# Kernel tuning notes

Measured on AMD Instinct MI355X. Metric: run time of the kernel, lower is better.

## Reference

```python
import jax, jax.numpy as jnp
import numpy as np

D_MODEL = 1024
N_HEADS = 16
HEAD_DIM = 64
SEQ = 2048
BATCH = 2
NEG = -1e9


def rotate_half(t):
    t1, t2 = jnp.split(t, 2, axis=-1)
    return jnp.concatenate([-t2, t1], axis=-1)


def setup_inputs() -> dict:
    key = jax.random.key(0)
    ks = jax.random.split(key, 7)
    std = 0.02
    x = jax.random.normal(ks[0], (BATCH, SEQ, D_MODEL), dtype=jnp.float32)
    # RoPE tables [seq_len, head_dim]
    inv_freq = 1.0 / (10000.0 ** (jnp.arange(0, HEAD_DIM, 2, dtype=jnp.float32) / HEAD_DIM))
    t = jnp.arange(SEQ, dtype=jnp.float32)
    freqs = jnp.outer(t, inv_freq)
    emb = jnp.concatenate([freqs, freqs], axis=-1)
    cos = jnp.cos(emb)
    sin = jnp.sin(emb)
    Wq = std * jax.random.normal(ks[1], (D_MODEL, D_MODEL), dtype=jnp.float32)
    Wk = std * jax.random.normal(ks[2], (D_MODEL, D_MODEL), dtype=jnp.float32)
    Wv = std * jax.random.normal(ks[3], (D_MODEL, D_MODEL), dtype=jnp.float32)
    Wo = std * jax.random.normal(ks[4], (D_MODEL, D_MODEL), dtype=jnp.float32)
    return {"x": x, "cos": cos, "sin": sin, "Wq": Wq, "Wk": Wk, "Wv": Wv, "Wo": Wo}


def reference(x, cos, sin, Wq, Wk, Wv, Wo):
    B, S, _ = x.shape
    scale = 1.0 / np.sqrt(HEAD_DIM)
    # projections (nn.Linear: y = x @ W.T)
    q = (x @ Wq.T).reshape(B, S, N_HEADS, HEAD_DIM).transpose(0, 2, 1, 3)  # [B,H,S,D]
    k = (x @ Wk.T).reshape(B, S, N_HEADS, HEAD_DIM).transpose(0, 2, 1, 3)
    v = (x @ Wv.T).reshape(B, S, N_HEADS, HEAD_DIM).transpose(0, 2, 1, 3)
    # RoPE
    c = cos[None, None, :, :]
    s = sin[None, None, :, :]
    q = q * c + rotate_half(q) * s
    k = k * c + rotate_half(k) * s
    # attention with additive causal mask
    scores = jnp.einsum('bhqd,bhkd->bhqk', q, k) * scale
    causal = jnp.triu(jnp.ones((S, S), dtype=jnp.float32), k=1) * NEG
    scores = scores + causal[None, None]
    attn = jax.nn.softmax(scores, axis=-1)
    out = jnp.einsum('bhqk,bhkd->bhqd', attn, v)
    out = out.transpose(0, 2, 1, 3).reshape(B, S, D_MODEL)
    return out @ Wo.T
```

## Files before the change

### kernel.cpp

```cpp
#include <hip/hip_runtime.h>
#include <hip/hip_bf16.h>
#include <math.h>

#define DM    1024
#define SEQL  2048
#define NB    2
#define MTOT  4096

typedef __attribute__((ext_vector_type(8))) short short8;
typedef __attribute__((ext_vector_type(4))) short short4v;
typedef __attribute__((ext_vector_type(4))) float float4v;

#define GLDS16(g, l) __builtin_amdgcn_global_load_lds( \
    (const __attribute__((address_space(1))) void*)(g), \
    (__attribute__((address_space(3))) void*)(l), 16, 0, 0)

__device__ __forceinline__ short f2bf(float f) {
  union { float f; unsigned u; } c; c.f = f;
  unsigned r = c.u + 0x7FFFu + ((c.u >> 16) & 1u);
  return (short)(r >> 16);
}

__global__ __launch_bounds__(256) void cvt_all(
    const float* __restrict__ x, const float* __restrict__ wq, const float* __restrict__ wk,
    const float* __restrict__ wv, const float* __restrict__ wo,
    short* __restrict__ xb, short* __restrict__ wqb, short* __restrict__ wkb,
    short* __restrict__ wvb, short* __restrict__ wob) {
  const int n4x = MTOT * DM / 4;
  int i = blockIdx.x * 256 + threadIdx.x;
  const float* s; short* d; int off;
  if (i < n4x) { s = x; d = xb; off = i; }
  else {
    int j = i - n4x;
    int sel = j >> 18;
    off = j & 0x3FFFF;
    s = (sel == 0) ? wq : (sel == 1) ? wk : (sel == 2) ? wv : wo;
    d = (sel == 0) ? wqb : (sel == 1) ? wkb : (sel == 2) ? wvb : wob;
  }
  float4 v = ((const float4*)s)[off];
  short4v o;
  o.x = f2bf(v.x); o.y = f2bf(v.y); o.z = f2bf(v.z); o.w = f2bf(v.w);
  ((short4v*)d)[off] = o;
}

template<int MODE>
__global__ __launch_bounds__(256, 2) void gemm_kernel(
    const short* __restrict__ A,
    const short* __restrict__ B0, const short* __restrict__ B1, const short* __restrict__ B2,
    void* __restrict__ out0, void* __restrict__ out1, void* __restrict__ out2,
    const float* __restrict__ cosp, const float* __restrict__ sinp)
{
  __shared__ short As[128 * 32];
  __shared__ short Bs[128 * 32];
  const int t = threadIdx.x;
  const int w = t >> 6, lane = t & 63;
  const int quad = lane >> 4, l16 = lane & 15;
  const int wm = w >> 1, wn = w & 1;
  const int bm = blockIdx.y * 128, bn = blockIdx.x * 128;

  const short* Bw;
  if (MODE == 2) Bw = B0;
  else Bw = (blockIdx.z == 0) ? B0 : ((blockIdx.z == 1) ? B1 : B2);

  float4v acc[4][4];
#pragma unroll
  for (int i = 0; i < 4; ++i)
#pragma unroll
    for (int j = 0; j < 4; ++j) { float4v z = {0.f, 0.f, 0.f, 0.f}; acc[i][j] = z; }

  for (int k0 = 0; k0 < DM; k0 += 32) {
#pragma unroll
    for (int i = 0; i < 2; ++i) {
      const int c = i * 256 + t;
      const int row = c >> 2, kc = c & 3;
      GLDS16(A  + (size_t)(bm + row) * DM + k0 + kc * 8, As + (i * 256 + w * 64) * 8);
      GLDS16(Bw + (size_t)(bn + row) * DM + k0 + kc * 8, Bs + (i * 256 + w * 64) * 8);
    }
    __syncthreads();
    short8 af[4], bf[4];
#pragma unroll
    for (int mt = 0; mt < 4; ++mt) af[mt] = *(const short8*)&As[(wm * 64 + mt * 16 + l16) * 32 + quad * 8];
#pragma unroll
    for (int nt = 0; nt < 4; ++nt) bf[nt] = *(const short8*)&Bs[(wn * 64 + nt * 16 + l16) * 32 + quad * 8];
#pragma unroll
    for (int mt = 0; mt < 4; ++mt)
#pragma unroll
      for (int nt = 0; nt < 4; ++nt)
        acc[mt][nt] = __builtin_amdgcn_mfma_f32_16x16x32_bf16(af[mt], bf[nt], acc[mt][nt], 0, 0, 0);
    __syncthreads();
  }

  if (MODE == 2) {
    float* fo = (float*)out0;
#pragma unroll
    for (int mt = 0; mt < 4; ++mt)
#pragma unroll
      for (int nt = 0; nt < 4; ++nt)
#pragma unroll
        for (int r = 0; r < 4; ++r) {
          int grow = bm + wm * 64 + mt * 16 + quad * 4 + r;
          int gcol = bn + wn * 64 + nt * 16 + l16;
          fo[(size_t)grow * DM + gcol] = acc[mt][nt][r];
        }
  } else if (blockIdx.z < 2) {
    short* qo = (short*)((blockIdx.z == 0) ? out0 : out1);
    const float sc = (blockIdx.z == 0) ? 0.125f : 1.0f;
#pragma unroll
    for (int mt = 0; mt < 4; ++mt)
#pragma unroll
      for (int r = 0; r < 4; ++r) {
        int grow = bm + wm * 64 + mt * 16 + quad * 4 + r;
        int s = grow & (SEQL - 1);
        int base = grow * DM + bn + wn * 64;
#pragma unroll
        for (int nt = 0; nt < 2; ++nt) {
          int d1 = nt * 16 + l16;
          float q1 = acc[mt][nt][r], q2 = acc[mt][nt + 2][r];
          float c1 = cosp[s * 64 + d1] * sc,      s1 = sinp[s * 64 + d1] * sc;
          float c2 = cosp[s * 64 + 32 + d1] * sc, s2 = sinp[s * 64 + 32 + d1] * sc;
          qo[base + d1]      = f2bf(q1 * c1 - q2 * s1);
          qo[base + 32 + d1] = f2bf(q2 * c2 + q1 * s2);
        }
      }
  } else {
    short* vo = (short*)out2;
#pragma unroll
    for (int mt = 0; mt < 4; ++mt)
#pragma unroll
      for (int nt = 0; nt < 4; ++nt) {
        int gc = bn + wn * 64 + nt * 16 + l16;
        int g0 = bm + wm * 64 + mt * 16 + quad * 4;
        short4v pk;
#pragma unroll
        for (int r = 0; r < 4; ++r) pk[r] = f2bf(acc[mt][nt][r]);
        *(short4v*)&vo[(size_t)gc * MTOT + g0] = pk;
      }
  }
}

__device__ __forceinline__ void softmax_pv(
    float4v* __restrict__ sA, float* __restrict__ lrun, float4v* __restrict__ o,
    short* __restrict__ Pw, const short* __restrict__ Vs,
    int qt, int kt, bool maskit, int w, int quad, int l16)
{
#pragma unroll
  for (int r = 0; r < 4; ++r) {
    int qrow = qt * 64 + w * 16 + quad * 4 + r;
#pragma unroll
    for (int nt = 0; nt < 8; ++nt) {
      float p;
      if (maskit && (kt * 128 + nt * 16 + l16 > qrow)) p = 0.f;
      else p = __expf(sA[nt][r]);
      lrun[r] += p;
      Pw[(quad * 4 + r) * 136 + nt * 16 + l16] = f2bf(p);
    }
  }
#pragma unroll
  for (int kk = 0; kk < 4; ++kk) {
    short8 ap = *(const short8*)&Pw[l16 * 136 + kk * 32 + quad * 8];
#pragma unroll
    for (int nt = 0; nt < 4; ++nt) {
      int d = nt * 16 + l16;
      short8 bv = *(const short8*)&Vs[(d * 16 + ((kk * 4 + quad) ^ (d & 7))) * 8];
      o[nt] = __builtin_amdgcn_mfma_f32_16x16x32_bf16(ap, bv, o[nt], 0, 0, 0);
    }
  }
}

__global__ __launch_bounds__(256, 2) void attn_kernel(
    const short* __restrict__ Q, const short* __restrict__ K,
    const short* __restrict__ Vt, short* __restrict__ O)
{
  __shared__ short Ks[128 * 64];
  __shared__ short Vs[64 * 128];
  __shared__ short Pl[4 * 16 * 136];
  const int t = threadIdx.x;
  const int w = t >> 6, lane = t & 63;
  const int quad = lane >> 4, l16 = lane & 15;
  const int qtA = blockIdx.x;
  const int qtB = 31 - blockIdx.x;
  const int bh = blockIdx.y;
  const int b = bh >> 4, h = bh & 15;
  const int rowbase = b * SEQL;
  const int colbase = h * 64;
  const int nktA = (qtA >> 1) + 1;
  const int nktB = (qtB >> 1) + 1;
  short* Pw = &Pl[w * 16 * 136];

  short8 aqA[2], aqB[2];
#pragma unroll
  for (int kk = 0; kk < 2; ++kk) {
    int rA = rowbase + qtA * 64 + w * 16 + l16;
    int rB = rowbase + qtB * 64 + w * 16 + l16;
    aqA[kk] = *(const short8*)&Q[(size_t)rA * DM + colbase + kk * 32 + quad * 8];
    aqB[kk] = *(const short8*)&Q[(size_t)rB * DM + colbase + kk * 32 + quad * 8];
  }

  float4v oA[4], oB[4];
  float lA[4], lB[4];
#pragma unroll
  for (int j = 0; j < 4; ++j) {
    float4v z = {0.f, 0.f, 0.f, 0.f};
    oA[j] = z; oB[j] = z; lA[j] = 0.f; lB[j] = 0.f;
  }

  for (int kt = 0; kt < nktB; ++kt) {
    const bool actA = (kt < nktA);
    {
      const short* Kbase = K + (size_t)(rowbase + kt * 128) * DM + colbase;
      const short* Vbase = Vt + (size_t)colbase * MTOT + rowbase + kt * 128;
#pragma unroll
      for (int j = 0; j < 4; ++j) {
        int i = j * 256 + t;
        int n = i >> 3, c = (i & 7) ^ (n & 7);
        GLDS16(Kbase + (size_t)n * DM + c * 8, Ks + (j * 256 + w * 64) * 8);
      }
#pragma unroll
      for (int j = 0; j < 4; ++j) {
        int i = j * 256 + t;
        int d = i >> 4, c = (i & 15) ^ (d & 7);
        GLDS16(Vbase + (size_t)d * MTOT + c * 8, Vs + (j * 256 + w * 64) * 8);
      }
    }
    __syncthreads();

    float4v sAa[8], sAb[8];
#pragma unroll
    for (int j = 0; j < 8; ++j) { float4v z = {0.f, 0.f, 0.f, 0.f}; sAa[j] = z; sAb[j] = z; }
    if (actA) {
#pragma unroll
      for (int nt = 0; nt < 8; ++nt) {
        int n = nt * 16 + l16;
        short8 bk0 = *(const short8*)&Ks[(n * 8 + (quad ^ (n & 7))) * 8];
        short8 bk1 = *(const short8*)&Ks[(n * 8 + ((4 + quad) ^ (n & 7))) * 8];
        sAa[nt] = __builtin_amdgcn_mfma_f32_16x16x32_bf16(aqA[0], bk0, sAa[nt], 0, 0, 0);
        sAa[nt] = __builtin_amdgcn_mfma_f32_16x16x32_bf16(aqA[1], bk1, sAa[nt], 0, 0, 0);
        sAb[nt] = __builtin_amdgcn_mfma_f32_16x16x32_bf16(aqB[0], bk0, sAb[nt], 0, 0, 0);
        sAb[nt] = __builtin_amdgcn_mfma_f32_16x16x32_bf16(aqB[1], bk1, sAb[nt], 0, 0, 0);
      }
    } else {
#pragma unroll
      for (int nt = 0; nt < 8; ++nt) {
        int n = nt * 16 + l16;
        short8 bk0 = *(const short8*)&Ks[(n * 8 + (quad ^ (n & 7))) * 8];
        short8 bk1 = *(const short8*)&Ks[(n * 8 + ((4 + quad) ^ (n & 7))) * 8];
        sAb[nt] = __builtin_amdgcn_mfma_f32_16x16x32_bf16(aqB[0], bk0, sAb[nt], 0, 0, 0);
        sAb[nt] = __builtin_amdgcn_mfma_f32_16x16x32_bf16(aqB[1], bk1, sAb[nt], 0, 0, 0);
      }
    }

    if (actA) softmax_pv(sAa, lA, oA, Pw, Vs, qtA, kt, kt == nktA - 1, w, quad, l16);
    softmax_pv(sAb, lB, oB, Pw, Vs, qtB, kt, kt == nktB - 1, w, quad, l16);
    __syncthreads();
  }

#pragma unroll
  for (int r = 0; r < 4; ++r) {
#pragma unroll
    for (int off = 1; off < 16; off <<= 1) {
      lA[r] += __shfl_xor(lA[r], off);
      lB[r] += __shfl_xor(lB[r], off);
    }
  }
#pragma unroll
  for (int nt = 0; nt < 4; ++nt)
#pragma unroll
    for (int r = 0; r < 4; ++r) {
      int gcol = colbase + nt * 16 + l16;
      int growA = rowbase + qtA * 64 + w * 16 + quad * 4 + r;
      int growB = rowbase + qtB * 64 + w * 16 + quad * 4 + r;
      O[(size_t)growA * DM + gcol] = f2bf(oA[nt][r] / lA[r]);
      O[(size_t)growB * DM + gcol] = f2bf(oB[nt][r] / lB[r]);
    }
}

extern "C" void kernel_launch(void* const* d_in, const int* in_sizes, int n_in,
                              void* d_out, int out_size, void* d_ws, size_t ws_size,
                              hipStream_t stream) {
  const float* x    = (const float*)d_in[0];
  const float* cosp = (const float*)d_in[1];
  const float* sinp = (const float*)d_in[2];
  const float* Wq   = (const float*)d_in[3];
  const float* Wk   = (const float*)d_in[4];
  const float* Wv   = (const float*)d_in[5];
  const float* Wo   = (const float*)d_in[6];

  char* ws = (char*)d_ws;
  const size_t XB = (size_t)MTOT * DM * 2;
  const size_t WB = (size_t)DM * DM * 2;
  short* xb    = (short*)(ws);
  short* wqb   = (short*)(ws + XB);
  short* wkb   = (short*)(ws + XB + 1 * WB);
  short* wvb   = (short*)(ws + XB + 2 * WB);
  short* wob   = (short*)(ws + XB + 3 * WB);
  short* Qb    = (short*)(ws + XB + 4 * WB);
  short* Kb    = (short*)(ws + XB + 4 * WB + XB);
  short* Vtb   = (short*)(ws + XB + 4 * WB + 2 * XB);
  short* attnb = xb;

  const int n4tot = (MTOT * DM + 4 * DM * DM) / 4;
  hipLaunchKernelGGL(cvt_all, dim3(n4tot / 256), dim3(256), 0, stream,
                     x, Wq, Wk, Wv, Wo, xb, wqb, wkb, wvb, wob);

  hipLaunchKernelGGL((gemm_kernel<0>), dim3(DM / 128, MTOT / 128, 3), dim3(256), 0, stream,
                     xb, wqb, wkb, wvb, (void*)Qb, (void*)Kb, (void*)Vtb, cosp, sinp);

  hipLaunchKernelGGL(attn_kernel, dim3(16, NB * 16), dim3(256), 0, stream,
                     Qb, Kb, Vtb, attnb);

  hipLaunchKernelGGL((gemm_kernel<2>), dim3(DM / 128, MTOT / 128, 1), dim3(256), 0, stream,
                     attnb, wob, wob, wob, d_out, nullptr, nullptr, cosp, sinp);
}
```

Before: 190.4 us.

## Keep softmax probabilities in registers, use exp2 scaling, split output GEMM tiles

The attention kernel computes S transposed (K as the A operand) so that each lane holds probabilities for its own query column. It packs them to bf16 in registers and feeds them straight into a 16x16x16 MFMA against V, dropping the LDS round-trip for P and one sync per tile. The Q scale folds in log2(e) so exp2 replaces expf, and the row sum becomes a single scalar reduced with two shuffles. The output projection gets its own kernel with 128x64 tiles to double the block count, and the QKV GEMM raises its occupancy hint to 3. The packbf helper rounds half-up instead of round-to-nearest-even, a small numerical difference.

```diff
diff --git a/kernel.cpp b/kernel.cpp
--- a/kernel.cpp
+++ b/kernel.cpp
@@ -19,6 +19,11 @@
   union { float f; unsigned u; } c; c.f = f;
   unsigned r = c.u + 0x7FFFu + ((c.u >> 16) & 1u);
   return (short)(r >> 16);
+}
+
+__device__ __forceinline__ int packbf(float a, float b) {
+  union { float f; unsigned u; } ca, cb; ca.f = a; cb.f = b;
+  return (int)__builtin_amdgcn_perm(cb.u + 0x8000u, ca.u + 0x8000u, 0x07060302u);
 }
 
 __global__ __launch_bounds__(256) void cvt_all(
@@ -43,11 +48,10 @@
   ((short4v*)d)[off] = o;
 }
 
-template<int MODE>
-__global__ __launch_bounds__(256, 2) void gemm_kernel(
+__global__ __launch_bounds__(256, 3) void qkv_kernel(
     const short* __restrict__ A,
     const short* __restrict__ B0, const short* __restrict__ B1, const short* __restrict__ B2,
-    void* __restrict__ out0, void* __restrict__ out1, void* __restrict__ out2,
+    short* __restrict__ out0, short* __restrict__ out1, short* __restrict__ out2,
     const float* __restrict__ cosp, const float* __restrict__ sinp)
 {
   __shared__ short As[128 * 32];
@@ -58,9 +62,7 @@
   const int wm = w >> 1, wn = w & 1;
   const int bm = blockIdx.y * 128, bn = blockIdx.x * 128;
 
-  const short* Bw;
-  if (MODE == 2) Bw = B0;
-  else Bw = (blockIdx.z == 0) ? B0 : ((blockIdx.z == 1) ? B1 : B2);
+  const short* Bw = (blockIdx.z == 0) ? B0 : ((blockIdx.z == 1) ? B1 : B2);
 
   float4v acc[4][4];
 #pragma unroll
@@ -90,21 +92,9 @@
     __syncthreads();
   }
 
-  if (MODE == 2) {
-    float* fo = (float*)out0;
-#pragma unroll
-    for (int mt = 0; mt < 4; ++mt)
-#pragma unroll
-      for (int nt = 0; nt < 4; ++nt)
-#pragma unroll
-        for (int r = 0; r < 4; ++r) {
-          int grow = bm + wm * 64 + mt * 16 + quad * 4 + r;
-          int gcol = bn + wn * 64 + nt * 16 + l16;
-          fo[(size_t)grow * DM + gcol] = acc[mt][nt][r];
-        }
-  } else if (blockIdx.z < 2) {
-    short* qo = (short*)((blockIdx.z == 0) ? out0 : out1);
-    const float sc = (blockIdx.z == 0) ? 0.125f : 1.0f;
+  if (blockIdx.z < 2) {
+    short* qo = (blockIdx.z == 0) ? out0 : out1;
+    const float sc = (blockIdx.z == 0) ? 0.18033688011112042f : 1.0f;
 #pragma unroll
     for (int mt = 0; mt < 4; ++mt)
 #pragma unroll
@@ -123,7 +113,7 @@
         }
       }
   } else {
-    short* vo = (short*)out2;
+    short* vo = out2;
 #pragma unroll
     for (int mt = 0; mt < 4; ++mt)
 #pragma unroll
@@ -138,34 +128,12 @@
   }
 }
 
-__device__ __forceinline__ void softmax_pv(
-    float4v* __restrict__ sA, float* __restrict__ lrun, float4v* __restrict__ o,
-    short* __restrict__ Pw, const short* __restrict__ Vs,
-    int qt, int kt, bool maskit, int w, int quad, int l16)
-{
-#pragma unroll
-  for (int r = 0; r < 4; ++r) {
-    int qrow = qt * 64 + w * 16 + quad * 4 + r;
-#pragma unroll
-    for (int nt = 0; nt < 8; ++nt) {
-      float p;
-      if (maskit && (kt * 128 + nt * 16 + l16 > qrow)) p = 0.f;
-      else p = __expf(sA[nt][r]);
-      lrun[r] += p;
-      Pw[(quad * 4 + r) * 136 + nt * 16 + l16] = f2bf(p);
-    }
-  }
-#pragma unroll
-  for (int kk = 0; kk < 4; ++kk) {
-    short8 ap = *(const short8*)&Pw[l16 * 136 + kk * 32 + quad * 8];
-#pragma unroll
-    for (int nt = 0; nt < 4; ++nt) {
-      int d = nt * 16 + l16;
-      short8 bv = *(const short8*)&Vs[(d * 16 + ((kk * 4 + quad) ^ (d & 7))) * 8];
-      o[nt] = __builtin_amdgcn_mfma_f32_16x16x32_bf16(ap, bv, o[nt], 0, 0, 0);
-    }
-  }
-}
+#if __has_builtin(__builtin_amdgcn_mfma_f32_16x16x16bf16_1k)
+#define HAVE_MFMA16 1
+#define MFMA16(a, b, c) __builtin_amdgcn_mfma_f32_16x16x16bf16_1k(a, b, c, 0, 0, 0)
+#else
+#define HAVE_MFMA16 0
+#endif
 
 __global__ __launch_bounds__(256, 2) void attn_kernel(
     const short* __restrict__ Q, const short* __restrict__ K,
@@ -173,7 +141,6 @@
 {
   __shared__ short Ks[128 * 64];
   __shared__ short Vs[64 * 128];
-  __shared__ short Pl[4 * 16 * 136];
   const int t = threadIdx.x;
   const int w = t >> 6, lane = t & 63;
   const int quad = lane >> 4, l16 = lane & 15;
@@ -185,27 +152,24 @@
   const int colbase = h * 64;
   const int nktA = (qtA >> 1) + 1;
   const int nktB = (qtB >> 1) + 1;
-  short* Pw = &Pl[w * 16 * 136];
+  const int qA = qtA * 64 + w * 16 + l16;
+  const int qB = qtB * 64 + w * 16 + l16;
 
   short8 aqA[2], aqB[2];
 #pragma unroll
   for (int kk = 0; kk < 2; ++kk) {
-    int rA = rowbase + qtA * 64 + w * 16 + l16;
-    int rB = rowbase + qtB * 64 + w * 16 + l16;
-    aqA[kk] = *(const short8*)&Q[(size_t)rA * DM + colbase + kk * 32 + quad * 8];
-    aqB[kk] = *(const short8*)&Q[(size_t)rB * DM + colbase + kk * 32 + quad * 8];
-  }
-
-  float4v oA[4], oB[4];
-  float lA[4], lB[4];
-#pragma unroll
-  for (int j = 0; j < 4; ++j) {
-    float4v z = {0.f, 0.f, 0.f, 0.f};
-    oA[j] = z; oB[j] = z; lA[j] = 0.f; lB[j] = 0.f;
-  }
+    aqA[kk] = *(const short8*)&Q[(size_t)(rowbase + qA) * DM + colbase + kk * 32 + quad * 8];
+    aqB[kk] = *(const short8*)&Q[(size_t)(rowbase + qB) * DM + colbase + kk * 32 + quad * 8];
+  }
+
+  float4v odA[4], odB[4];
+#pragma unroll
+  for (int j = 0; j < 4; ++j) { float4v z = {0.f, 0.f, 0.f, 0.f}; odA[j] = z; odB[j] = z; }
+  float lA = 0.f, lB = 0.f;
 
   for (int kt = 0; kt < nktB; ++kt) {
     const bool actA = (kt < nktA);
+    const bool diagA = (kt == nktA - 1), diagB = (kt == nktB - 1);
     {
       const short* Kbase = K + (size_t)(rowbase + kt * 128) * DM + colbase;
       const short* Vbase = Vt + (size_t)colbase * MTOT + rowbase + kt * 128;
@@ -224,54 +188,146 @@
     }
     __syncthreads();
 
-    float4v sAa[8], sAb[8];
-#pragma unroll
-    for (int j = 0; j < 8; ++j) { float4v z = {0.f, 0.f, 0.f, 0.f}; sAa[j] = z; sAb[j] = z; }
-    if (actA) {
-#pragma unroll
-      for (int nt = 0; nt < 8; ++nt) {
-        int n = nt * 16 + l16;
-        short8 bk0 = *(const short8*)&Ks[(n * 8 + (quad ^ (n & 7))) * 8];
-        short8 bk1 = *(const short8*)&Ks[(n * 8 + ((4 + quad) ^ (n & 7))) * 8];
-        sAa[nt] = __builtin_amdgcn_mfma_f32_16x16x32_bf16(aqA[0], bk0, sAa[nt], 0, 0, 0);
-        sAa[nt] = __builtin_amdgcn_mfma_f32_16x16x32_bf16(aqA[1], bk1, sAa[nt], 0, 0, 0);
-        sAb[nt] = __builtin_amdgcn_mfma_f32_16x16x32_bf16(aqB[0], bk0, sAb[nt], 0, 0, 0);
-        sAb[nt] = __builtin_amdgcn_mfma_f32_16x16x32_bf16(aqB[1], bk1, sAb[nt], 0, 0, 0);
-      }
-    } else {
-#pragma unroll
-      for (int nt = 0; nt < 8; ++nt) {
-        int n = nt * 16 + l16;
-        short8 bk0 = *(const short8*)&Ks[(n * 8 + (quad ^ (n & 7))) * 8];
-        short8 bk1 = *(const short8*)&Ks[(n * 8 + ((4 + quad) ^ (n & 7))) * 8];
-        sAb[nt] = __builtin_amdgcn_mfma_f32_16x16x32_bf16(aqB[0], bk0, sAb[nt], 0, 0, 0);
-        sAb[nt] = __builtin_amdgcn_mfma_f32_16x16x32_bf16(aqB[1], bk1, sAb[nt], 0, 0, 0);
-      }
-    }
-
-    if (actA) softmax_pv(sAa, lA, oA, Pw, Vs, qtA, kt, kt == nktA - 1, w, quad, l16);
-    softmax_pv(sAb, lB, oB, Pw, Vs, qtB, kt, kt == nktB - 1, w, quad, l16);
-    __syncthreads();
-  }
-
-#pragma unroll
-  for (int r = 0; r < 4; ++r) {
-#pragma unroll
-    for (int off = 1; off < 16; off <<= 1) {
-      lA[r] += __shfl_xor(lA[r], off);
-      lB[r] += __shfl_xor(lB[r], off);
-    }
-  }
-#pragma unroll
-  for (int nt = 0; nt < 4; ++nt)
-#pragma unroll
-    for (int r = 0; r < 4; ++r) {
-      int gcol = colbase + nt * 16 + l16;
-      int growA = rowbase + qtA * 64 + w * 16 + quad * 4 + r;
-      int growB = rowbase + qtB * 64 + w * 16 + quad * 4 + r;
-      O[(size_t)growA * DM + gcol] = f2bf(oA[nt][r] / lA[r]);
-      O[(size_t)growB * DM + gcol] = f2bf(oB[nt][r] / lB[r]);
-    }
+    int pkA[8][2], pkB[8][2];
+#pragma unroll
+    for (int nt = 0; nt < 8; ++nt) {
+      int n = nt * 16 + l16;
+      short8 bk0 = *(const short8*)&Ks[(n * 8 + (quad ^ (n & 7))) * 8];
+      short8 bk1 = *(const short8*)&Ks[(n * 8 + ((4 + quad) ^ (n & 7))) * 8];
+      const int kb = kt * 128 + nt * 16 + quad * 4;
+      float4v zz = {0.f, 0.f, 0.f, 0.f};
+      float4v sB = __builtin_amdgcn_mfma_f32_16x16x32_bf16(bk0, aqB[0], zz, 0, 0, 0);
+      sB = __builtin_amdgcn_mfma_f32_16x16x32_bf16(bk1, aqB[1], sB, 0, 0, 0);
+      float pb[4];
+#pragma unroll
+      for (int r = 0; r < 4; ++r) {
+        float p = (diagB && (kb + r > qB)) ? 0.f : __builtin_amdgcn_exp2f(sB[r]);
+        lB += p; pb[r] = p;
+      }
+      pkB[nt][0] = packbf(pb[0], pb[1]);
+      pkB[nt][1] = packbf(pb[2], pb[3]);
+      if (actA) {
+        float4v sA = __builtin_amdgcn_mfma_f32_16x16x32_bf16(bk0, aqA[0], zz, 0, 0, 0);
+        sA = __builtin_amdgcn_mfma_f32_16x16x32_bf16(bk1, aqA[1], sA, 0, 0, 0);
+        float pa[4];
+#pragma unroll
+        for (int r = 0; r < 4; ++r) {
+          float p = (diagA && (kb + r > qA)) ? 0.f : __builtin_amdgcn_exp2f(sA[r]);
+          lA += p; pa[r] = p;
+        }
+        pkA[nt][0] = packbf(pa[0], pa[1]);
+        pkA[nt][1] = packbf(pa[2], pa[3]);
+      }
+    }
+
+#if HAVE_MFMA16
+#pragma unroll
+    for (int kk = 0; kk < 8; ++kk) {
+      union { int i[2]; short4v s; } ubB, ubA;
+      ubB.i[0] = pkB[kk][0]; ubB.i[1] = pkB[kk][1];
+      if (actA) { ubA.i[0] = pkA[kk][0]; ubA.i[1] = pkA[kk][1]; }
+#pragma unroll
+      for (int dt = 0; dt < 4; ++dt) {
+        int d = dt * 16 + l16;
+        short4v av = *(const short4v*)&Vs[(d * 16 + ((kk * 2 + (quad >> 1)) ^ (d & 7))) * 8 + (quad & 1) * 4];
+        odB[dt] = MFMA16(av, ubB.s, odB[dt]);
+        if (actA) odA[dt] = MFMA16(av, ubA.s, odA[dt]);
+      }
+    }
+#else
+#pragma unroll
+    for (int kk = 0; kk < 4; ++kk) {
+      union { int i[4]; short8 s; } ubB, ubA;
+#pragma unroll
+      for (int dj = 0; dj < 4; ++dj) {
+        int src = (((quad & 1) * 2 + (dj >> 1)) << 4) + l16;
+        int b0 = __shfl(pkB[2 * kk][dj & 1], src);
+        int b1 = __shfl(pkB[2 * kk + 1][dj & 1], src);
+        ubB.i[dj] = (quad >= 2) ? b1 : b0;
+        int a0 = __shfl(pkA[2 * kk][dj & 1], src);
+        int a1 = __shfl(pkA[2 * kk + 1][dj & 1], src);
+        ubA.i[dj] = (quad >= 2) ? a1 : a0;
+      }
+#pragma unroll
+      for (int dt = 0; dt < 4; ++dt) {
+        int d = dt * 16 + l16;
+        short8 av = *(const short8*)&Vs[(d * 16 + ((kk * 4 + quad) ^ (d & 7))) * 8];
+        odB[dt] = __builtin_amdgcn_mfma_f32_16x16x32_bf16(av, ubB.s, odB[dt], 0, 0, 0);
+        if (actA) odA[dt] = __builtin_amdgcn_mfma_f32_16x16x32_bf16(av, ubA.s, odA[dt], 0, 0, 0);
+      }
+    }
+#endif
+    __syncthreads();
+  }
+
+  lA += __shfl_xor(lA, 16); lA += __shfl_xor(lA, 32);
+  lB += __shfl_xor(lB, 16); lB += __shfl_xor(lB, 32);
+  const float iA = 1.f / lA, iB = 1.f / lB;
+
+#pragma unroll
+  for (int dt = 0; dt < 4; ++dt) {
+    short4v sa, sb;
+#pragma unroll
+    for (int r = 0; r < 4; ++r) { sa[r] = f2bf(odA[dt][r] * iA); sb[r] = f2bf(odB[dt][r] * iB); }
+    int col = colbase + dt * 16 + quad * 4;
+    *(short4v*)&O[(size_t)(rowbase + qA) * DM + col] = sa;
+    *(short4v*)&O[(size_t)(rowbase + qB) * DM + col] = sb;
+  }
+}
+
+__global__ __launch_bounds__(256, 2) void gemm_out(
+    const short* __restrict__ A, const short* __restrict__ B,
+    float* __restrict__ out)
+{
+  __shared__ short As[128 * 32];
+  __shared__ short Bs[64 * 32];
+  const int t = threadIdx.x;
+  const int w = t >> 6, lane = t & 63;
+  const int quad = lane >> 4, l16 = lane & 15;
+  const int wm = w >> 1, wn = w & 1;
+  const int bm = blockIdx.y * 128, bn = blockIdx.x * 64;
+
+  float4v acc[4][2];
+#pragma unroll
+  for (int i = 0; i < 4; ++i)
+#pragma unroll
+    for (int j = 0; j < 2; ++j) { float4v z = {0.f, 0.f, 0.f, 0.f}; acc[i][j] = z; }
+
+  for (int k0 = 0; k0 < DM; k0 += 32) {
+#pragma unroll
+    for (int i = 0; i < 2; ++i) {
+      const int c = i * 256 + t;
+      const int row = c >> 2, kc = c & 3;
+      GLDS16(A + (size_t)(bm + row) * DM + k0 + kc * 8, As + (i * 256 + w * 64) * 8);
+    }
+    {
+      const int row = t >> 2, kc = t & 3;
+      GLDS16(B + (size_t)(bn + row) * DM + k0 + kc * 8, Bs + (w * 64) * 8);
+    }
+    __syncthreads();
+    short8 af[4], bf[2];
+#pragma unroll
+    for (int mt = 0; mt < 4; ++mt) af[mt] = *(const short8*)&As[(wm * 64 + mt * 16 + l16) * 32 + quad * 8];
+#pragma unroll
+    for (int nt = 0; nt < 2; ++nt) bf[nt] = *(const short8*)&Bs[(wn * 32 + nt * 16 + l16) * 32 + quad * 8];
+#pragma unroll
+    for (int mt = 0; mt < 4; ++mt)
+#pragma unroll
+      for (int nt = 0; nt < 2; ++nt)
+        acc[mt][nt] = __builtin_amdgcn_mfma_f32_16x16x32_bf16(af[mt], bf[nt], acc[mt][nt], 0, 0, 0);
+    __syncthreads();
+  }
+
+#pragma unroll
+  for (int mt = 0; mt < 4; ++mt)
+#pragma unroll
+    for (int nt = 0; nt < 2; ++nt)
+#pragma unroll
+      for (int r = 0; r < 4; ++r) {
+        int grow = bm + wm * 64 + mt * 16 + quad * 4 + r;
+        int gcol = bn + wn * 32 + nt * 16 + l16;
+        out[(size_t)grow * DM + gcol] = acc[mt][nt][r];
+      }
 }
 
 extern "C" void kernel_launch(void* const* d_in, const int* in_sizes, int n_in,
@@ -302,12 +358,12 @@
   hipLaunchKernelGGL(cvt_all, dim3(n4tot / 256), dim3(256), 0, stream,
                      x, Wq, Wk, Wv, Wo, xb, wqb, wkb, wvb, wob);
 
-  hipLaunchKernelGGL((gemm_kernel<0>), dim3(DM / 128, MTOT / 128, 3), dim3(256), 0, stream,
-                     xb, wqb, wkb, wvb, (void*)Qb, (void*)Kb, (void*)Vtb, cosp, sinp);
+  hipLaunchKernelGGL(qkv_kernel, dim3(DM / 128, MTOT / 128, 3), dim3(256), 0, stream,
+                     xb, wqb, wkb, wvb, Qb, Kb, Vtb, cosp, sinp);
 
   hipLaunchKernelGGL(attn_kernel, dim3(16, NB * 16), dim3(256), 0, stream,
                      Qb, Kb, Vtb, attnb);
 
-  hipLaunchKernelGGL((gemm_kernel<2>), dim3(DM / 128, MTOT / 128, 1), dim3(256), 0, stream,
-                     attnb, wob, wob, wob, d_out, nullptr, nullptr, cosp, sinp);
-}
+  hipLaunchKernelGGL(gemm_out, dim3(DM / 64, MTOT / 128), dim3(256), 0, stream,
+                     attnb, wob, (float*)d_out);
+}
```

New measurement: 200.9 us. 1.06x slower.
